# Kernel tuning notes

Measured on AMD Instinct MI355X. Metric: run time of the kernel, lower is better.

## Reference

```python
import jax, jax.numpy as jnp
import numpy as np

LATENT, HIDDEN = 512, 1024


def _gru_cell(x, h, w_ih, w_hh, b_ih, b_hh):
    # PyTorch GRU cell: gates ordered (r, z, n)
    gi = x @ w_ih.T + b_ih          # (B, 3H)
    gh = h @ w_hh.T + b_hh          # (B, 3H)
    i_r, i_z, i_n = jnp.split(gi, 3, axis=-1)
    h_r, h_z, h_n = jnp.split(gh, 3, axis=-1)
    r = jax.nn.sigmoid(i_r + h_r)
    z = jax.nn.sigmoid(i_z + h_z)
    n = jnp.tanh(i_n + r * h_n)
    return (1.0 - z) * n + z * h


def setup_inputs() -> dict:
    key = jax.random.key(0)
    ks = jax.random.split(key, 16)
    B, T_in = 128, 64
    k = 1.0 / np.sqrt(HIDDEN)
    u = lambda kk, shape: jax.random.uniform(kk, shape, jnp.float32, -k, k)
    return {
        "context_latents": jax.random.normal(ks[0], (B, T_in, LATENT), jnp.float32),
        "w_ih_l0": u(ks[1], (3 * HIDDEN, LATENT)),
        "w_hh_l0": u(ks[2], (3 * HIDDEN, HIDDEN)),
        "b_ih_l0": u(ks[3], (3 * HIDDEN,)),
        "b_hh_l0": u(ks[4], (3 * HIDDEN,)),
        "w_ih_l1": u(ks[5], (3 * HIDDEN, HIDDEN)),
        "w_hh_l1": u(ks[6], (3 * HIDDEN, HIDDEN)),
        "b_ih_l1": u(ks[7], (3 * HIDDEN,)),
        "b_hh_l1": u(ks[8], (3 * HIDDEN,)),
        "w1": u(ks[9], (HIDDEN, HIDDEN)),
        "bp1": u(ks[10], (HIDDEN,)),
        "w2": u(ks[11], (LATENT, HIDDEN)),
        "bp2": u(ks[12], (LATENT,)),
        "num_predictions": 64,
    }


def reference(context_latents, w_ih_l0, w_hh_l0, b_ih_l0, b_hh_l0,
              w_ih_l1, w_hh_l1, b_ih_l1, b_hh_l1, w1, bp1, w2, bp2,
              num_predictions):
    B = context_latents.shape[0]
    h0 = jnp.zeros((B, HIDDEN), context_latents.dtype)
    h1 = jnp.zeros((B, HIDDEN), context_latents.dtype)

    def stack(x_t, h0, h1):
        h0 = _gru_cell(x_t, h0, w_ih_l0, w_hh_l0, b_ih_l0, b_hh_l0)
        h1 = _gru_cell(h0, h1, w_ih_l1, w_hh_l1, b_ih_l1, b_hh_l1)
        return h0, h1

    # Encode context: scan over time (B, T_in, D) -> final hidden states
    def enc_step(carry, x_t):
        h0, h1 = carry
        h0, h1 = stack(x_t, h0, h1)
        return (h0, h1), None

    (h0, h1), _ = jax.lax.scan(enc_step, (h0, h1),
                               jnp.swapaxes(context_latents, 0, 1))

    def dec_step(carry, _):
        h0, h1, x = carry
        h0, h1 = stack(x, h0, h1)
        y = jax.nn.relu(h1 @ w1.T + bp1) @ w2.T + bp2   # (B, LATENT)
        return (h0, h1, y), y

    x0 = context_latents[:, -1, :]
    _, ys = jax.lax.scan(dec_step, (h0, h1, x0), None, length=num_predictions)
    return jnp.swapaxes(ys, 0, 1)  # (B, T_out, LATENT)
```

## Files before the change

### kernel.cpp

```cpp
#include <hip/hip_runtime.h>
#include <math.h>

#define B 128
#define LATENT 512
#define H 1024
#define BH (B * H)

typedef unsigned short ushort_t;
typedef unsigned int uint_t;
typedef __bf16 bf16x8 __attribute__((ext_vector_type(8)));
typedef float f32x4 __attribute__((ext_vector_type(4)));


__global__ __launch_bounds__(256) void zero4_kernel(float4* __restrict__ p, int n4) {
  int i = blockIdx.x * blockDim.x + threadIdx.x;
  int stride = gridDim.x * blockDim.x;
  float4 z = {0.f, 0.f, 0.f, 0.f};
  for (; i < n4; i += stride) p[i] = z;
}

__device__ __forceinline__ void split_bf16(float f, ushort_t& h, ushort_t& l) {
  uint_t u = __float_as_uint(f);
  uint_t hb = (u + 0x7FFFu + ((u >> 16) & 1u)) >> 16;
  float fh = __uint_as_float(hb << 16);
  float r = f - fh;
  uint_t v = __float_as_uint(r);
  uint_t lb = (v + 0x7FFFu + ((v >> 16) & 1u)) >> 16;
  h = (ushort_t)hb; l = (ushort_t)lb;
}

__global__ __launch_bounds__(256) void split_kernel(const float* __restrict__ src,
                                                    ushort_t* __restrict__ hi,
                                                    ushort_t* __restrict__ lo, int n) {
  int i = blockIdx.x * blockDim.x + threadIdx.x;
  int stride = gridDim.x * blockDim.x;
  for (; i < n; i += stride) {
    ushort_t h, l;
    split_bf16(src[i], h, l);
    hi[i] = h; lo[i] = l;
  }
}

__global__ __launch_bounds__(256) void split_hi_kernel(const float* __restrict__ src,
                                                       ushort_t* __restrict__ hi, int n) {
  int i = blockIdx.x * blockDim.x + threadIdx.x;
  int stride = gridDim.x * blockDim.x;
  for (; i < n; i += stride) {
    uint_t u = __float_as_uint(src[i]);
    hi[i] = (ushort_t)((u + 0x7FFFu + ((u >> 16) & 1u)) >> 16);
  }
}

__global__ __launch_bounds__(256) void wf_kernel(const float* __restrict__ wih0,
                                                 const float* __restrict__ w2,
                                                 ushort_t* __restrict__ wfh,
                                                 ushort_t* __restrict__ wfl) {
  __shared__ float As[32][33];
  __shared__ float Bs[32][33];
  const int i0 = blockIdx.x * 32;
  const int k0 = blockIdx.y * 32;
  const int tid = threadIdx.x;
  const int r = tid >> 3, c4 = (tid & 7) << 2;
  float acc[4] = {0.f, 0.f, 0.f, 0.f};
  for (int m0 = 0; m0 < LATENT; m0 += 32) {
    {
      const float4 v = *reinterpret_cast<const float4*>(&wih0[(size_t)(i0 + r) * LATENT + m0 + c4]);
      As[r][c4] = v.x; As[r][c4 + 1] = v.y; As[r][c4 + 2] = v.z; As[r][c4 + 3] = v.w;
      const float4 w = *reinterpret_cast<const float4*>(&w2[(size_t)(m0 + r) * H + k0 + c4]);
      Bs[r][c4] = w.x; Bs[r][c4 + 1] = w.y; Bs[r][c4 + 2] = w.z; Bs[r][c4 + 3] = w.w;
    }
    __syncthreads();
    #pragma unroll
    for (int mm = 0; mm < 32; ++mm) {
      const float a = As[r][mm];
      #pragma unroll
      for (int x = 0; x < 4; ++x) acc[x] = fmaf(a, Bs[mm][c4 + x], acc[x]);
    }
    __syncthreads();
  }
  #pragma unroll
  for (int x = 0; x < 4; ++x) {
    ushort_t h, l;
    split_bf16(acc[x], h, l);
    const size_t o = (size_t)(i0 + r) * H + k0 + c4 + x;
    wfh[o] = h; wfl[o] = l;
  }
}

__global__ __launch_bounds__(256) void bias_fuse_kernel(const float* __restrict__ wih0,
                                                        const float* __restrict__ bp2,
                                                        const float* __restrict__ bih0,
                                                        float* __restrict__ bf0) {
  int g = blockIdx.x * blockDim.x + threadIdx.x;
  if (g < 3 * H) {
    float s = bih0[g];
    const float* row = wih0 + (size_t)g * LATENT;
    #pragma unroll 4
    for (int l = 0; l < LATENT; ++l) s = fmaf(row[l], bp2[l], s);
    bf0[g] = s;
  }
}

__device__ __forceinline__ float sigmoidf_(float v) { return 1.0f / (1.0f + expf(-v)); }

__device__ __forceinline__ void grid_barrier(unsigned* bar, int tid, int bid) {
  __syncthreads();
  if (tid == 0) {
    const int g = bid & 7;
    unsigned* arr    = bar + (g << 6);
    unsigned* rel    = bar + 1024 + (g << 6);
    unsigned* master = bar + 2048;
    unsigned gen = __hip_atomic_load(rel, __ATOMIC_RELAXED, __HIP_MEMORY_SCOPE_AGENT);
    unsigned a = __hip_atomic_fetch_add(arr, 1u, __ATOMIC_ACQ_REL, __HIP_MEMORY_SCOPE_AGENT);
    if (a == 31u) {
      __hip_atomic_store(arr, 0u, __ATOMIC_RELAXED, __HIP_MEMORY_SCOPE_AGENT);
      unsigned m = __hip_atomic_fetch_add(master, 1u, __ATOMIC_ACQ_REL, __HIP_MEMORY_SCOPE_AGENT);
      if (m == 7u) {
        __hip_atomic_store(master, 0u, __ATOMIC_RELAXED, __HIP_MEMORY_SCOPE_AGENT);
        #pragma unroll
        for (int i = 0; i < 8; ++i)
          __hip_atomic_fetch_add(bar + 1024 + (i << 6), 1u, __ATOMIC_ACQ_REL, __HIP_MEMORY_SCOPE_AGENT);
      }
    }
    while (__hip_atomic_load(rel, __ATOMIC_RELAXED, __HIP_MEMORY_SCOPE_AGENT) == gen)
      __builtin_amdgcn_s_sleep(1);
    (void)__hip_atomic_load(rel, __ATOMIC_ACQUIRE, __HIP_MEMORY_SCOPE_AGENT);
  }
  __syncthreads();
}

template <int NJ, int NG, int PH, int EPI, bool WLO>
__device__ __forceinline__ void phase_mm(
    char* smem, const int tid, const int Mb, const int jb, const bool active,
    const ushort_t* aAh, const ushort_t* aAl, int aApitch, int K1,
    const ushort_t* wAh, const ushort_t* wAl,
    const ushort_t* aBh, const ushort_t* aBl, int aBpitch, int K2,
    const ushort_t* wBh,
    const float* bih, const float* bhh,
    const float* h_prev, float* h_out,
    ushort_t* out_hi, ushort_t* out_lo, int split_pitch,
    const float* bias, float* out_f32)
{
  if (!active) return;
  constexpr int NW = NJ * NG;
  constexpr int NSLOTA = 4 + NW * (WLO ? 2 : 1);
  constexpr int NSLOTB = 4 + NW;
  constexpr int BUFB = NSLOTA * 4096;
  constexpr int NPG = PH * NW;
  constexpr int CW = NJ * 16;

  const int b0 = Mb * 32;
  const int j0 = jb * CW;
  const int NC1 = K1 >> 7;
  const int NC2 = (PH == 2) ? (K2 >> 7) : 0;
  const int NC = NC1 + NC2;

  const char* g[NSLOTA];
  auto build = [&](const ushort_t* ah, const ushort_t* al, int apitch,
                   const ushort_t* wh, const ushort_t* wl, int K) {
    const int rowt = tid >> 4;
    const int cp = tid & 15;
    const int cc = cp ^ rowt;
    #pragma unroll
    for (int u = 0; u < NSLOTA; ++u) {
      const ushort_t* basep; size_t off;
      if (u < 2)      { basep = ah; off = (size_t)(b0 + u * 16 + rowt) * apitch + cc * 8; }
      else if (u < 4) { basep = al; off = (size_t)(b0 + (u - 2) * 16 + rowt) * apitch + cc * 8; }
      else if (u < 4 + NW) {
        const int w = u - 4, jt = w % NJ, gate = w / NJ;
        const int wrow = (NG == 3) ? (gate * H + j0 + jt * 16 + rowt) : (j0 + jt * 16 + rowt);
        basep = wh; off = (size_t)wrow * K + cc * 8;
      } else {
        const int w = u - 4 - NW, jt = w % NJ, gate = w / NJ;
        const int wrow = (NG == 3) ? (gate * H + j0 + jt * 16 + rowt) : (j0 + jt * 16 + rowt);
        basep = (wl != nullptr) ? wl : wh; off = (size_t)wrow * K + cc * 8;
      }
      g[u] = (const char*)(basep + off);
    }
  };

  const int s = tid >> 6;
  const int q = (tid >> 4) & 3;
  const int r = tid & 15;
  const int gs = (((4 * s + q) ^ r) << 4);
  const int offA00 = r * 256 + gs;
  const int offA01 = 4096 + r * 256 + gs;
  const int offA10 = 8192 + r * 256 + gs;
  const int offA11 = 12288 + r * 256 + gs;
  int offWh[NW];
  int offWl[NW];
  #pragma unroll
  for (int w = 0; w < NW; ++w) {
    offWh[w] = (4 + w) * 4096 + r * 256 + gs;
    offWl[w] = (4 + NW + w) * 4096 + r * 256 + gs;
  }

  f32x4 accA[NJ][NG][2];
  f32x4 accB[NJ][NG][2];
  #pragma unroll
  for (int jt = 0; jt < NJ; ++jt)
    #pragma unroll
    for (int gg = 0; gg < NG; ++gg)
      #pragma unroll
      for (int mf = 0; mf < 2; ++mf) {
        accA[jt][gg][mf] = (f32x4){0.f, 0.f, 0.f, 0.f};
        accB[jt][gg][mf] = (f32x4){0.f, 0.f, 0.f, 0.f};
      }

  const unsigned wofs = (unsigned)(tid >> 6) * 1024;
  auto issue = [&](int bsel, int koff, int nslot) {
    #pragma unroll
    for (int u = 0; u < NSLOTA; ++u) {
      if (u < nslot) {
        __builtin_amdgcn_global_load_lds(
            (const __attribute__((address_space(1))) void*)(g[u] + koff),
            (__attribute__((address_space(3))) void*)(smem + bsel * BUFB + u * 4096 + wofs),
            16, 0, 0);
      }
    }
  };

  auto computeA = [&](int bsel) {
    const char* base = smem + bsel * BUFB;
    bf16x8 ah0 = *(const bf16x8*)(base + offA00);
    bf16x8 ah1 = *(const bf16x8*)(base + offA01);
    bf16x8 al0 = *(const bf16x8*)(base + offA10);
    bf16x8 al1 = *(const bf16x8*)(base + offA11);
    #pragma unroll
    for (int gg = 0; gg < NG; ++gg)
      #pragma unroll
      for (int jt = 0; jt < NJ; ++jt) {
        const int w = gg * NJ + jt;
        bf16x8 wh = *(const bf16x8*)(base + offWh[w]);
        accA[jt][gg][0] = __builtin_amdgcn_mfma_f32_16x16x32_bf16(ah0, wh, accA[jt][gg][0], 0, 0, 0);
        if (WLO) {
          bf16x8 wl = *(const bf16x8*)(base + offWl[w]);
          accA[jt][gg][0] = __builtin_amdgcn_mfma_f32_16x16x32_bf16(ah0, wl, accA[jt][gg][0], 0, 0, 0);
          accA[jt][gg][1] = __builtin_amdgcn_mfma_f32_16x16x32_bf16(ah1, wl, accA[jt][gg][1], 0, 0, 0);
        }
        accA[jt][gg][0] = __builtin_amdgcn_mfma_f32_16x16x32_bf16(al0, wh, accA[jt][gg][0], 0, 0, 0);
        accA[jt][gg][1] = __builtin_amdgcn_mfma_f32_16x16x32_bf16(ah1, wh, accA[jt][gg][1], 0, 0, 0);
        accA[jt][gg][1] = __builtin_amdgcn_mfma_f32_16x16x32_bf16(al1, wh, accA[jt][gg][1], 0, 0, 0);
      }
  };
  auto computeB = [&](int bsel) {
    const char* base = smem + bsel * BUFB;
    bf16x8 ah0 = *(const bf16x8*)(base + offA00);
    bf16x8 ah1 = *(const bf16x8*)(base + offA01);
    bf16x8 al0 = *(const bf16x8*)(base + offA10);
    bf16x8 al1 = *(const bf16x8*)(base + offA11);
    #pragma unroll
    for (int gg = 0; gg < NG; ++gg)
      #pragma unroll
      for (int jt = 0; jt < NJ; ++jt) {
        const int w = gg * NJ + jt;
        bf16x8 wh = *(const bf16x8*)(base + offWh[w]);
        accB[jt][gg][0] = __builtin_amdgcn_mfma_f32_16x16x32_bf16(ah0, wh, accB[jt][gg][0], 0, 0, 0);
        accB[jt][gg][0] = __builtin_amdgcn_mfma_f32_16x16x32_bf16(al0, wh, accB[jt][gg][0], 0, 0, 0);
        accB[jt][gg][1] = __builtin_amdgcn_mfma_f32_16x16x32_bf16(ah1, wh, accB[jt][gg][1], 0, 0, 0);
        accB[jt][gg][1] = __builtin_amdgcn_mfma_f32_16x16x32_bf16(al1, wh, accB[jt][gg][1], 0, 0, 0);
      }
  };

  build(aAh, aAl, aApitch, wAh, wAl, K1);
  issue(0, 0, NSLOTA);

  #pragma unroll 1
  for (int c = 0; c < NC; ++c) {
    __syncthreads();
    if (c + 1 < NC) {
      if (PH == 2 && c + 1 == NC1) {
        build(aBh, aBl, aBpitch, wBh, nullptr, K2);
        issue((c + 1) & 1, 0, NSLOTB);
      } else {
        const bool isB = (PH == 2) && (c + 1 >= NC1);
        const int koff = (isB ? (c + 1 - NC1) : (c + 1)) * 256;
        issue((c + 1) & 1, koff, isB ? NSLOTB : NSLOTA);
      }
    }
    if (PH == 1 || c < NC1) computeA(c & 1);
    else                    computeB(c & 1);
  }
  __syncthreads();

  const int lane = tid & 63;
  #pragma unroll
  for (int gg = 0; gg < NG; ++gg)
    #pragma unroll
    for (int jt = 0; jt < NJ; ++jt)
      #pragma unroll
      for (int mf = 0; mf < 2; ++mf) {
        const int w = gg * NJ + jt;
        *(f32x4*)(smem + (size_t)(((s * NPG + w) * 2 + mf) * 64 + lane) * 16) = accA[jt][gg][mf];
        if (PH == 2)
          *(f32x4*)(smem + (size_t)(((s * NPG + NW + w) * 2 + mf) * 64 + lane) * 16) = accB[jt][gg][mf];
      }
  __syncthreads();

  for (int o = tid; o < 32 * CW; o += 256) {
    const int row = o / CW, c = o % CW;
    const int jt = c >> 4, cr = c & 15;
    const int mf = row >> 4, br = row & 15, qq = br >> 2, rg = br & 3;
    const int ln = cr + qq * 16;
    float v[PH * NG];
    #pragma unroll
    for (int pg = 0; pg < PH * NG; ++pg) {
      const int w = (pg < NG) ? (pg * NJ + jt) : (NW + (pg - NG) * NJ + jt);
      float sum = 0.f;
      #pragma unroll
      for (int ss = 0; ss < 4; ++ss)
        sum += *(const float*)(smem + (size_t)(((ss * NPG + w) * 2 + mf) * 64 + ln) * 16 + rg * 4);
      v[pg] = sum;
    }
    const int bglob = b0 + row, jglob = j0 + c;
// ... 6 lines not shown
      float hn = v[5] + bhh[2 * H + jglob];
      float rr_ = sigmoidf_(ir + hr);
      float zz_ = sigmoidf_(iz + hz);
      float nn_ = tanhf(in_ + rr_ * hn);
      float hp = h_prev[(size_t)bglob * H + jglob];
      float ho = (1.f - zz_) * nn_ + zz_ * hp;
      h_out[(size_t)bglob * H + jglob] = ho;
      ushort_t hb, lb;
      split_bf16(ho, hb, lb);
      out_hi[(size_t)bglob * H + jglob] = hb;
      out_lo[(size_t)bglob * H + jglob] = lb;
    } else if (EPI == 1) {
      float vv = v[0] + bias[jglob];
      vv = fmaxf(vv, 0.f);
      ushort_t hb, lb;
      split_bf16(vv, hb, lb);
      out_hi[(size_t)bglob * split_pitch + jglob] = hb;
      out_lo[(size_t)bglob * split_pitch + jglob] = lb;
    } else {
      float vv = v[0] + bias[jglob];
      const int tt = bglob >> 7, bb2 = bglob & 127;
      out_f32[((size_t)bb2 * split_pitch + tt) * LATENT + jglob] = vv;
    }
  }
  __syncthreads();
}


struct PParams {
  const ushort_t *ctxh, *ctxl;
  const ushort_t *wih0h, *whh0h;
  const ushort_t *wih1h, *whh1h;
  const ushort_t *w1h;
  const ushort_t *wfh, *wfl;
  const float *bih0, *bhh0, *bih1, *bhh1, *bp1;
  const float *bf0;
  float *h0f0, *h0f1, *h1f0, *h1f1;
  ushort_t *h0hi0, *h0lo0, *h0hi1, *h0lo1;
  ushort_t *h1hi0, *h1lo0, *h1hi1, *h1lo1;
  ushort_t *h0Ahi, *h0Alo;
  unsigned* bar;
  int T_in, n_pred, ctx_pitch;
};

__global__ __launch_bounds__(256, 1) void gru_persistent(PParams P) {
  __shared__ char smem[98304];
  const int tid = threadIdx.x;
  const int bid = blockIdx.x;

  float* h0f[2] = {P.h0f0, P.h0f1};
  float* h1f[2] = {P.h1f0, P.h1f1};
  ushort_t* h0hi[2] = {P.h0hi0, P.h0hi1};
  ushort_t* h0lo[2] = {P.h0lo0, P.h0lo1};
  ushort_t* h1hi[2] = {P.h1hi0, P.h1hi1};
  ushort_t* h1lo[2] = {P.h1lo0, P.h1lo1};

  int p0 = 0, p1 = 0;

  const int idx = (bid < 128) ? bid : (bid - 128);
  const int eMb = idx & 3;
  const int ejb = idx >> 2;
  #pragma unroll 1
  for (int p = 0; p <= P.T_in; ++p) {
    const int n0 = p0 ^ 1, n1 = p1 ^ 1;
    if (bid < 128) {
      if (p < P.T_in) {
        const int t = p;
        phase_mm<2, 3, 2, 0, false>(smem, tid, eMb, ejb, true,
            P.ctxh + (size_t)t * LATENT, P.ctxl + (size_t)t * LATENT, P.ctx_pitch, LATENT,
            P.wih0h, nullptr,
            (t == 0) ? P.h0hi0 : P.h0Ahi + (size_t)(t - 1) * BH,
            (t == 0) ? P.h0lo0 : P.h0Alo + (size_t)(t - 1) * BH, H, H, P.whh0h,
            P.bih0, P.bhh0, h0f[p0], h0f[n0],
            P.h0Ahi + (size_t)t * BH, P.h0Alo + (size_t)t * BH, H, nullptr, nullptr);
      }
    } else {
      if (p >= 1) {
        const int t = p - 1;
        phase_mm<2, 3, 2, 0, false>(smem, tid, eMb, ejb, true,
            P.h0Ahi + (size_t)t * BH, P.h0Alo + (size_t)t * BH, H, H,
            P.wih1h, nullptr,
            h1hi[p1], h1lo[p1], H, H, P.whh1h,
            P.bih1, P.bhh1, h1f[p1], h1f[n1],
            h1hi[n1], h1lo[n1], H, nullptr, nullptr);
      }
    }
    grid_barrier(P.bar, tid, bid);
    if (p < P.T_in) p0 = n0;
    if (p >= 1) p1 = n1;
  }

  const int dMb = bid & 3;
  const int djb = bid >> 2;
  const ushort_t* d0ph = P.h0Ahi + (size_t)(P.T_in - 1) * BH;
  const ushort_t* d0pl = P.h0Alo + (size_t)(P.T_in - 1) * BH;
  ushort_t* pAh = P.h0Ahi;
  ushort_t* pAl = P.h0Alo;
  #pragma unroll 1
  for (int t = 0; t < P.n_pred; ++t) {
    const int n0 = p0 ^ 1;
    if (t == 0) {
      phase_mm<1, 3, 2, 0, false>(smem, tid, dMb, djb, true,
          P.ctxh + (size_t)(P.T_in - 1) * LATENT, P.ctxl + (size_t)(P.T_in - 1) * LATENT,
          P.ctx_pitch, LATENT,
          P.wih0h, nullptr,
          d0ph, d0pl, H, H, P.whh0h,
          P.bih0, P.bhh0, h0f[p0], h0f[n0], h0hi[n0], h0lo[n0], H, nullptr, nullptr);
    } else {
      phase_mm<1, 3, 2, 0, true>(smem, tid, dMb, djb, true,
          pAh + (size_t)(t - 1) * BH, pAl + (size_t)(t - 1) * BH, H, H,
          P.wfh, P.wfl,
          d0ph, d0pl, H, H, P.whh0h,
          P.bf0, P.bhh0, h0f[p0], h0f[n0], h0hi[n0], h0lo[n0], H, nullptr, nullptr);
    }
    grid_barrier(P.bar, tid, bid);
    d0ph = h0hi[n0]; d0pl = h0lo[n0];
    const int n1 = p1 ^ 1;
    phase_mm<1, 3, 2, 0, false>(smem, tid, dMb, djb, true,
        h0hi[n0], h0lo[n0], H, H,
        P.wih1h, nullptr,
        h1hi[p1], h1lo[p1], H, H, P.whh1h,
        P.bih1, P.bhh1, h1f[p1], h1f[n1], h1hi[n1], h1lo[n1], H, nullptr, nullptr);
    grid_barrier(P.bar, tid, bid);
    phase_mm<1, 1, 1, 1, false>(smem, tid, dMb, djb, true,
        h1hi[n1], h1lo[n1], H, H,
        P.w1h, nullptr,
        nullptr, nullptr, 0, 0, nullptr,
        nullptr, nullptr, nullptr, nullptr,
        pAh + (size_t)t * BH, pAl + (size_t)t * BH, H, P.bp1, nullptr);
    grid_barrier(P.bar, tid, bid);
    p0 = n0; p1 = n1;
  }
}

__global__ __launch_bounds__(256, 2) void proj_out_kernel(
    const ushort_t* __restrict__ pAh, const ushort_t* __restrict__ pAl,
    const ushort_t* __restrict__ w2h, const float* __restrict__ bp2,
    float* __restrict__ out, int n_pred)
{
  __shared__ char smem[49152];
  const int tid = threadIdx.x;
  const int rt = blockIdx.x >> 4;
  const int ct = blockIdx.x & 15;
  phase_mm<2, 1, 1, 3, false>(smem, tid, rt, ct, true,
      pAh, pAl, H, H,
      w2h, nullptr,
      nullptr, nullptr, 0, 0, nullptr,
      nullptr, nullptr, nullptr, nullptr,
      nullptr, nullptr, n_pred, bp2, out);
}


__global__ __launch_bounds__(256) void gru_cell_kernel(
    const float* __restrict__ x, int xs, int Kih,
    const float* __restrict__ h_prev,
    const float* __restrict__ wih, const float* __restrict__ whh,
    const float* __restrict__ bih, const float* __restrict__ bhh,
    float* __restrict__ h_out)
{
  __shared__ float Xs[32][33];
  __shared__ float Ws[48][33];
  const int tid = threadIdx.x;
  const int b0 = blockIdx.x * 32;
  const int j0 = blockIdx.y * 16;
  const int bg = tid & 15;
  const int jj = tid >> 4;
  const int j = j0 + jj;
  float accA[2][3];
  float accB[2][3];
  #pragma unroll
  for (int g = 0; g < 3; ++g) {
    const float bi = bih[g * H + j];
    const float bh = bhh[g * H + j];
    accA[0][g] = bi; accA[1][g] = bi;
    accB[0][g] = bh; accB[1][g] = bh;
  }
  for (int k0 = 0; k0 < Kih; k0 += 32) {
    {
      const int rr = tid >> 3, c4 = (tid & 7) << 2;
// ... 116 lines not shown
  const float* bhh0 = (const float*)d_in[4];
  const float* wih1 = (const float*)d_in[5];
  const float* whh1 = (const float*)d_in[6];
  const float* bih1 = (const float*)d_in[7];
  const float* bhh1 = (const float*)d_in[8];
  const float* w1   = (const float*)d_in[9];
  const float* bp1  = (const float*)d_in[10];
  const float* w2   = (const float*)d_in[11];
  const float* bp2  = (const float*)d_in[12];

  const int T_in   = in_sizes[0] / (B * LATENT);
  const int n_pred = out_size / (B * LATENT);
  float* out = (float*)d_out;

  size_t cur = 0;
  auto alloc = [&](size_t bytes) -> void* {
    void* p = (char*)d_ws + cur;
    cur += (bytes + 255) & ~(size_t)255;
    return p;
  };
  const int E_wih0 = 3 * H * LATENT, E_whh0 = 3 * H * H;
  const int E_wih1 = 3 * H * H, E_whh1 = 3 * H * H;
  const int E_w1 = H * H, E_w2 = LATENT * H;
  const int E_wf = 3 * H * H;
  const int E_ctx = in_sizes[0];

  ushort_t* wih0h = (ushort_t*)alloc(E_wih0 * 2);
  ushort_t* whh0h = (ushort_t*)alloc(E_whh0 * 2);
  ushort_t* wih1h = (ushort_t*)alloc(E_wih1 * 2);
  ushort_t* whh1h = (ushort_t*)alloc(E_whh1 * 2);
  ushort_t* w1h   = (ushort_t*)alloc(E_w1 * 2);
  ushort_t* w2h   = (ushort_t*)alloc(E_w2 * 2);
  ushort_t* wfh   = (ushort_t*)alloc((size_t)E_wf * 2);
  ushort_t* wfl   = (ushort_t*)alloc((size_t)E_wf * 2);
  ushort_t* ctxh  = (ushort_t*)alloc((size_t)E_ctx * 2);
  ushort_t* ctxl  = (ushort_t*)alloc((size_t)E_ctx * 2);
  ushort_t* h0Ahi = (ushort_t*)alloc((size_t)T_in * BH * 2);
  ushort_t* h0Alo = (ushort_t*)alloc((size_t)T_in * BH * 2);
  float* bf0 = (float*)alloc(3 * H * 4);
  size_t zero_start = cur;
  float* h0f[2]; float* h1f[2];
  ushort_t* h0hi[2]; ushort_t* h0lo[2]; ushort_t* h1hi[2]; ushort_t* h1lo[2];
  h0f[0] = (float*)alloc(BH * 4); h0f[1] = (float*)alloc(BH * 4);
  h1f[0] = (float*)alloc(BH * 4); h1f[1] = (float*)alloc(BH * 4);
  h0hi[0] = (ushort_t*)alloc(BH * 2); h0lo[0] = (ushort_t*)alloc(BH * 2);
  h0hi[1] = (ushort_t*)alloc(BH * 2); h0lo[1] = (ushort_t*)alloc(BH * 2);
  h1hi[0] = (ushort_t*)alloc(BH * 2); h1lo[0] = (ushort_t*)alloc(BH * 2);
  h1hi[1] = (ushort_t*)alloc(BH * 2); h1lo[1] = (ushort_t*)alloc(BH * 2);
  unsigned* bar = (unsigned*)alloc(16384);
  size_t zero_bytes = cur - zero_start;
  size_t required = cur;

  if (ws_size >= required && n_pred <= T_in) {
    auto splitA = [&](const float* s, ushort_t* hi, ushort_t* lo, int n) {
      int blocks = (n + 255) / 256; if (blocks > 2048) blocks = 2048;
      split_kernel<<<blocks, 256, 0, stream>>>(s, hi, lo, n);
    };
    auto splitW = [&](const float* s, ushort_t* hi, int n) {
      int blocks = (n + 255) / 256; if (blocks > 2048) blocks = 2048;
      split_hi_kernel<<<blocks, 256, 0, stream>>>(s, hi, n);
    };
    splitW(wih0, wih0h, E_wih0);
    splitW(whh0, whh0h, E_whh0);
    splitW(wih1, wih1h, E_wih1);
    splitW(whh1, whh1h, E_whh1);
    splitW(w1, w1h, E_w1);
    splitW(w2, w2h, E_w2);
    wf_kernel<<<dim3(3 * H / 32, H / 32), 256, 0, stream>>>(wih0, w2, wfh, wfl);
    bias_fuse_kernel<<<(3 * H + 255) / 256, 256, 0, stream>>>(wih0, bp2, bih0, bf0);
    splitA(ctx, ctxh, ctxl, E_ctx);
    {
      int n4 = (int)(zero_bytes / 16);
      zero4_kernel<<<2048, 256, 0, stream>>>((float4*)((char*)d_ws + zero_start), n4);
    }

    PParams P;
    P.ctxh = ctxh; P.ctxl = ctxl;
    P.wih0h = wih0h; P.whh0h = whh0h;
    P.wih1h = wih1h; P.whh1h = whh1h;
    P.w1h = w1h; P.wfh = wfh; P.wfl = wfl;
    P.bih0 = bih0; P.bhh0 = bhh0; P.bih1 = bih1; P.bhh1 = bhh1; P.bp1 = bp1;
    P.bf0 = bf0;
    P.h0f0 = h0f[0]; P.h0f1 = h0f[1]; P.h1f0 = h1f[0]; P.h1f1 = h1f[1];
    P.h0hi0 = h0hi[0]; P.h0lo0 = h0lo[0]; P.h0hi1 = h0hi[1]; P.h0lo1 = h0lo[1];
    P.h1hi0 = h1hi[0]; P.h1lo0 = h1lo[0]; P.h1hi1 = h1hi[1]; P.h1lo1 = h1lo[1];
    P.h0Ahi = h0Ahi; P.h0Alo = h0Alo;
    P.bar = bar;
    P.T_in = T_in; P.n_pred = n_pred; P.ctx_pitch = T_in * LATENT;

    gru_persistent<<<256, 256, 0, stream>>>(P);

    const int rowtiles = (n_pred * B) / 32;
    proj_out_kernel<<<rowtiles * 16, 256, 0, stream>>>(h0Ahi, h0Alo, w2h, bp2, out, n_pred);
    return;
  }

  float* ws = (float*)d_ws;
  float* h0a = ws;
  float* h0b = h0a + (size_t)BH;
  float* h1a = h0b + (size_t)BH;
  float* h1b = h1a + (size_t)BH;
  float* p   = h1b + (size_t)BH;
  {
    int n4 = (4 * BH) / 4;
    zero4_kernel<<<256, 256, 0, stream>>>((float4*)h0a, n4);
  }
  float* y = p + (size_t)BH;
  float* h0p = h0a; float* h0n = h0b;
  float* h1p = h1a; float* h1n = h1b;
  const dim3 cgrid(4, 64);
  for (int t = 0; t < T_in; ++t) {
    const float* x = ctx + (size_t)t * LATENT;
    gru_cell_kernel<<<cgrid, 256, 0, stream>>>(x, T_in * LATENT, LATENT,
// ... 27 lines not shown
```

Baseline: 6.677 ms.

## Widen decode K-chunks to 256 and drop low-part fused weight

Adds a CHUNKW template parameter so the decoder-phase matmuls stage 256-wide K chunks per pipeline step instead of 128. This halves the number of load/sync iterations per phase and grows the shared buffer to fit. It also removes the bf16 low half of the fused wih0·w2 weight, so layer-0 decode steps issue fewer MFMAs and load less data. The cost is lower precision in the fused-weight path and higher LDS use per block.

```diff
diff --git a/kernel.cpp b/kernel.cpp
--- a/kernel.cpp
+++ b/kernel.cpp
@@ -53,8 +53,7 @@
 
 __global__ __launch_bounds__(256) void wf_kernel(const float* __restrict__ wih0,
                                                  const float* __restrict__ w2,
-                                                 ushort_t* __restrict__ wfh,
-                                                 ushort_t* __restrict__ wfl) {
+                                                 ushort_t* __restrict__ wfh) {
   __shared__ float As[32][33];
   __shared__ float Bs[32][33];
   const int i0 = blockIdx.x * 32;
@@ -80,10 +79,9 @@
   }
   #pragma unroll
   for (int x = 0; x < 4; ++x) {
-    ushort_t h, l;
-    split_bf16(acc[x], h, l);
-    const size_t o = (size_t)(i0 + r) * H + k0 + c4 + x;
-    wfh[o] = h; wfl[o] = l;
+    uint_t u = __float_as_uint(acc[x]);
+    wfh[(size_t)(i0 + r) * H + k0 + c4 + x] =
+        (ushort_t)((u + 0x7FFFu + ((u >> 16) & 1u)) >> 16);
   }
 }
 
@@ -129,7 +127,7 @@
   __syncthreads();
 }
 
-template <int NJ, int NG, int PH, int EPI, bool WLO>
+template <int NJ, int NG, int PH, int EPI, bool WLO, int CHUNKW>
 __device__ __forceinline__ void phase_mm(
     char* smem, const int tid, const int Mb, const int jb, const bool active,
     const ushort_t* aAh, const ushort_t* aAl, int aApitch, int K1,
@@ -142,17 +140,20 @@
     const float* bias, float* out_f32)
 {
   if (!active) return;
+  constexpr int KST = CHUNKW / 128;
+  constexpr int SLOTB = CHUNKW * 32;
   constexpr int NW = NJ * NG;
   constexpr int NSLOTA = 4 + NW * (WLO ? 2 : 1);
   constexpr int NSLOTB = 4 + NW;
-  constexpr int BUFB = NSLOTA * 4096;
+  constexpr int BUFB = NSLOTA * SLOTB;
   constexpr int NPG = PH * NW;
   constexpr int CW = NJ * 16;
+  constexpr int CSHIFT = (CHUNKW == 256) ? 8 : 7;
 
   const int b0 = Mb * 32;
   const int j0 = jb * CW;
-  const int NC1 = K1 >> 7;
-  const int NC2 = (PH == 2) ? (K2 >> 7) : 0;
+  const int NC1 = K1 >> CSHIFT;
+  const int NC2 = (PH == 2) ? (K2 >> CSHIFT) : 0;
   const int NC = NC1 + NC2;
 
   const char* g[NSLOTA];
@@ -182,18 +183,13 @@
   const int s = tid >> 6;
   const int q = (tid >> 4) & 3;
   const int r = tid & 15;
-  const int gs = (((4 * s + q) ^ r) << 4);
-  const int offA00 = r * 256 + gs;
-  const int offA01 = 4096 + r * 256 + gs;
-  const int offA10 = 8192 + r * 256 + gs;
-  const int offA11 = 12288 + r * 256 + gs;
-  int offWh[NW];
-  int offWl[NW];
+  int gsv[KST];
   #pragma unroll
-  for (int w = 0; w < NW; ++w) {
-    offWh[w] = (4 + w) * 4096 + r * 256 + gs;
-    offWl[w] = (4 + NW + w) * 4096 + r * 256 + gs;
-  }
+  for (int k2 = 0; k2 < KST; ++k2) {
+    const int G = s * (4 * KST) + k2 * 4 + q;
+    gsv[k2] = (G >> 4) * 4096 + ((G & 15) ^ r) * 16;
+  }
+  const int rbase = r * 256;
 
   f32x4 accA[NJ][NG][2];
   f32x4 accB[NJ][NG][2];
@@ -212,54 +208,65 @@
     #pragma unroll
     for (int u = 0; u < NSLOTA; ++u) {
       if (u < nslot) {
-        __builtin_amdgcn_global_load_lds(
-            (const __attribute__((address_space(1))) void*)(g[u] + koff),
-            (__attribute__((address_space(3))) void*)(smem + bsel * BUFB + u * 4096 + wofs),
-            16, 0, 0);
+        #pragma unroll
+        for (int j = 0; j < KST; ++j) {
+          __builtin_amdgcn_global_load_lds(
+              (const __attribute__((address_space(1))) void*)(g[u] + koff + j * 256),
+              (__attribute__((address_space(3))) void*)(smem + bsel * BUFB + u * SLOTB + j * 4096 + wofs),
+              16, 0, 0);
+        }
       }
     }
   };
 
   auto computeA = [&](int bsel) {
     const char* base = smem + bsel * BUFB;
-    bf16x8 ah0 = *(const bf16x8*)(base + offA00);
-    bf16x8 ah1 = *(const bf16x8*)(base + offA01);
-    bf16x8 al0 = *(const bf16x8*)(base + offA10);
-    bf16x8 al1 = *(const bf16x8*)(base + offA11);
-    #pragma unroll
-    for (int gg = 0; gg < NG; ++gg)
+    #pragma unroll
+    for (int k2 = 0; k2 < KST; ++k2) {
+      const int fo = rbase + gsv[k2];
+      bf16x8 ah0 = *(const bf16x8*)(base + 0 * SLOTB + fo);
+      bf16x8 ah1 = *(const bf16x8*)(base + 1 * SLOTB + fo);
+      bf16x8 al0 = *(const bf16x8*)(base + 2 * SLOTB + fo);
+      bf16x8 al1 = *(const bf16x8*)(base + 3 * SLOTB + fo);
       #pragma unroll
-      for (int jt = 0; jt < NJ; ++jt) {
-        const int w = gg * NJ + jt;
-        bf16x8 wh = *(const bf16x8*)(base + offWh[w]);
-        accA[jt][gg][0] = __builtin_amdgcn_mfma_f32_16x16x32_bf16(ah0, wh, accA[jt][gg][0], 0, 0, 0);
-        if (WLO) {
-          bf16x8 wl = *(const bf16x8*)(base + offWl[w]);
-          accA[jt][gg][0] = __builtin_amdgcn_mfma_f32_16x16x32_bf16(ah0, wl, accA[jt][gg][0], 0, 0, 0);
-          accA[jt][gg][1] = __builtin_amdgcn_mfma_f32_16x16x32_bf16(ah1, wl, accA[jt][gg][1], 0, 0, 0);
+      for (int gg = 0; gg < NG; ++gg)
+        #pragma unroll
+        for (int jt = 0; jt < NJ; ++jt) {
+          const int w = gg * NJ + jt;
+          bf16x8 wh = *(const bf16x8*)(base + (4 + w) * SLOTB + fo);
+          accA[jt][gg][0] = __builtin_amdgcn_mfma_f32_16x16x32_bf16(ah0, wh, accA[jt][gg][0], 0, 0, 0);
+          if (WLO) {
+            bf16x8 wl = *(const bf16x8*)(base + (4 + NW + w) * SLOTB + fo);
+            accA[jt][gg][0] = __builtin_amdgcn_mfma_f32_16x16x32_bf16(ah0, wl, accA[jt][gg][0], 0, 0, 0);
+            accA[jt][gg][1] = __builtin_amdgcn_mfma_f32_16x16x32_bf16(ah1, wl, accA[jt][gg][1], 0, 0, 0);
+          }
+          accA[jt][gg][0] = __builtin_amdgcn_mfma_f32_16x16x32_bf16(al0, wh, accA[jt][gg][0], 0, 0, 0);
+          accA[jt][gg][1] = __builtin_amdgcn_mfma_f32_16x16x32_bf16(ah1, wh, accA[jt][gg][1], 0, 0, 0);
+          accA[jt][gg][1] = __builtin_amdgcn_mfma_f32_16x16x32_bf16(al1, wh, accA[jt][gg][1], 0, 0, 0);
         }
-        accA[jt][gg][0] = __builtin_amdgcn_mfma_f32_16x16x32_bf16(al0, wh, accA[jt][gg][0], 0, 0, 0);
-        accA[jt][gg][1] = __builtin_amdgcn_mfma_f32_16x16x32_bf16(ah1, wh, accA[jt][gg][1], 0, 0, 0);
-        accA[jt][gg][1] = __builtin_amdgcn_mfma_f32_16x16x32_bf16(al1, wh, accA[jt][gg][1], 0, 0, 0);
-      }
+    }
   };
   auto computeB = [&](int bsel) {
     const char* base = smem + bsel * BUFB;
-    bf16x8 ah0 = *(const bf16x8*)(base + offA00);
-    bf16x8 ah1 = *(const bf16x8*)(base + offA01);
-    bf16x8 al0 = *(const bf16x8*)(base + offA10);
-    bf16x8 al1 = *(const bf16x8*)(base + offA11);
-    #pragma unroll
-    for (int gg = 0; gg < NG; ++gg)
+    #pragma unroll
+    for (int k2 = 0; k2 < KST; ++k2) {
+      const int fo = rbase + gsv[k2];
+      bf16x8 ah0 = *(const bf16x8*)(base + 0 * SLOTB + fo);
+      bf16x8 ah1 = *(const bf16x8*)(base + 1 * SLOTB + fo);
+      bf16x8 al0 = *(const bf16x8*)(base + 2 * SLOTB + fo);
+      bf16x8 al1 = *(const bf16x8*)(base + 3 * SLOTB + fo);
       #pragma unroll
-      for (int jt = 0; jt < NJ; ++jt) {
-        const int w = gg * NJ + jt;
-        bf16x8 wh = *(const bf16x8*)(base + offWh[w]);
-        accB[jt][gg][0] = __builtin_amdgcn_mfma_f32_16x16x32_bf16(ah0, wh, accB[jt][gg][0], 0, 0, 0);
-        accB[jt][gg][0] = __builtin_amdgcn_mfma_f32_16x16x32_bf16(al0, wh, accB[jt][gg][0], 0, 0, 0);
-        accB[jt][gg][1] = __builtin_amdgcn_mfma_f32_16x16x32_bf16(ah1, wh, accB[jt][gg][1], 0, 0, 0);
-        accB[jt][gg][1] = __builtin_amdgcn_mfma_f32_16x16x32_bf16(al1, wh, accB[jt][gg][1], 0, 0, 0);
-      }
+      for (int gg = 0; gg < NG; ++gg)
+        #pragma unroll
+        for (int jt = 0; jt < NJ; ++jt) {
+          const int w = gg * NJ + jt;
+          bf16x8 wh = *(const bf16x8*)(base + (4 + w) * SLOTB + fo);
+          accB[jt][gg][0] = __builtin_amdgcn_mfma_f32_16x16x32_bf16(ah0, wh, accB[jt][gg][0], 0, 0, 0);
+          accB[jt][gg][0] = __builtin_amdgcn_mfma_f32_16x16x32_bf16(al0, wh, accB[jt][gg][0], 0, 0, 0);
+          accB[jt][gg][1] = __builtin_amdgcn_mfma_f32_16x16x32_bf16(ah1, wh, accB[jt][gg][1], 0, 0, 0);
+          accB[jt][gg][1] = __builtin_amdgcn_mfma_f32_16x16x32_bf16(al1, wh, accB[jt][gg][1], 0, 0, 0);
+        }
+    }
   };
 
   build(aAh, aAl, aApitch, wAh, wAl, K1);
@@ -274,7 +281,7 @@
         issue((c + 1) & 1, 0, NSLOTB);
       } else {
         const bool isB = (PH == 2) && (c + 1 >= NC1);
-        const int koff = (isB ? (c + 1 - NC1) : (c + 1)) * 256;
+        const int koff = (isB ? (c + 1 - NC1) : (c + 1)) * (CHUNKW * 2);
         issue((c + 1) & 1, koff, isB ? NSLOTB : NSLOTA);
       }
     }
@@ -352,7 +359,7 @@
   const ushort_t *wih0h, *whh0h;
   const ushort_t *wih1h, *whh1h;
   const ushort_t *w1h;
-  const ushort_t *wfh, *wfl;
+  const ushort_t *wfh;
   const float *bih0, *bhh0, *bih1, *bhh1, *bp1;
   const float *bf0;
   float *h0f0, *h0f1, *h1f0, *h1f1;
@@ -364,7 +371,7 @@
 };
 
 __global__ __launch_bounds__(256, 1) void gru_persistent(PParams P) {
-  __shared__ char smem[98304];
+  __shared__ char smem[114688];
   const int tid = threadIdx.x;
   const int bid = blockIdx.x;
 
@@ -386,7 +393,7 @@
     if (bid < 128) {
       if (p < P.T_in) {
         const int t = p;
-        phase_mm<2, 3, 2, 0, false>(smem, tid, eMb, ejb, true,
+        phase_mm<2, 3, 2, 0, false, 128>(smem, tid, eMb, ejb, true,
             P.ctxh + (size_t)t * LATENT, P.ctxl + (size_t)t * LATENT, P.ctx_pitch, LATENT,
             P.wih0h, nullptr,
             (t == 0) ? P.h0hi0 : P.h0Ahi + (size_t)(t - 1) * BH,
@@ -397,7 +404,7 @@
     } else {
       if (p >= 1) {
         const int t = p - 1;
-        phase_mm<2, 3, 2, 0, false>(smem, tid, eMb, ejb, true,
+        phase_mm<2, 3, 2, 0, false, 128>(smem, tid, eMb, ejb, true,
             P.h0Ahi + (size_t)t * BH, P.h0Alo + (size_t)t * BH, H, H,
             P.wih1h, nullptr,
             h1hi[p1], h1lo[p1], H, H, P.whh1h,
@@ -420,29 +427,29 @@
   for (int t = 0; t < P.n_pred; ++t) {
     const int n0 = p0 ^ 1;
     if (t == 0) {
-      phase_mm<1, 3, 2, 0, false>(smem, tid, dMb, djb, true,
+      phase_mm<1, 3, 2, 0, false, 256>(smem, tid, dMb, djb, true,
           P.ctxh + (size_t)(P.T_in - 1) * LATENT, P.ctxl + (size_t)(P.T_in - 1) * LATENT,
           P.ctx_pitch, LATENT,
           P.wih0h, nullptr,
           d0ph, d0pl, H, H, P.whh0h,
           P.bih0, P.bhh0, h0f[p0], h0f[n0], h0hi[n0], h0lo[n0], H, nullptr, nullptr);
     } else {
-      phase_mm<1, 3, 2, 0, true>(smem, tid, dMb, djb, true,
+      phase_mm<1, 3, 2, 0, false, 256>(smem, tid, dMb, djb, true,
           pAh + (size_t)(t - 1) * BH, pAl + (size_t)(t - 1) * BH, H, H,
-          P.wfh, P.wfl,
+          P.wfh, nullptr,
           d0ph, d0pl, H, H, P.whh0h,
           P.bf0, P.bhh0, h0f[p0], h0f[n0], h0hi[n0], h0lo[n0], H, nullptr, nullptr);
     }
     grid_barrier(P.bar, tid, bid);
     d0ph = h0hi[n0]; d0pl = h0lo[n0];
     const int n1 = p1 ^ 1;
-    phase_mm<1, 3, 2, 0, false>(smem, tid, dMb, djb, true,
+    phase_mm<1, 3, 2, 0, false, 256>(smem, tid, dMb, djb, true,
         h0hi[n0], h0lo[n0], H, H,
         P.wih1h, nullptr,
         h1hi[p1], h1lo[p1], H, H, P.whh1h,
         P.bih1, P.bhh1, h1f[p1], h1f[n1], h1hi[n1], h1lo[n1], H, nullptr, nullptr);
     grid_barrier(P.bar, tid, bid);
-    phase_mm<1, 1, 1, 1, false>(smem, tid, dMb, djb, true,
+    phase_mm<1, 1, 1, 1, false, 256>(smem, tid, dMb, djb, true,
         h1hi[n1], h1lo[n1], H, H,
         P.w1h, nullptr,
         nullptr, nullptr, 0, 0, nullptr,
@@ -462,7 +469,7 @@
   const int tid = threadIdx.x;
   const int rt = blockIdx.x >> 4;
   const int ct = blockIdx.x & 15;
-  phase_mm<2, 1, 1, 3, false>(smem, tid, rt, ct, true,
+  phase_mm<2, 1, 1, 3, false, 128>(smem, tid, rt, ct, true,
       pAh, pAl, H, H,
       w2h, nullptr,
       nullptr, nullptr, 0, 0, nullptr,
@@ -647,7 +654,6 @@
   ushort_t* w1h   = (ushort_t*)alloc(E_w1 * 2);
   ushort_t* w2h   = (ushort_t*)alloc(E_w2 * 2);
   ushort_t* wfh   = (ushort_t*)alloc((size_t)E_wf * 2);
-  ushort_t* wfl   = (ushort_t*)alloc((size_t)E_wf * 2);
   ushort_t* ctxh  = (ushort_t*)alloc((size_t)E_ctx * 2);
   ushort_t* ctxl  = (ushort_t*)alloc((size_t)E_ctx * 2);
   ushort_t* h0Ahi = (ushort_t*)alloc((size_t)T_in * BH * 2);
@@ -681,7 +687,7 @@
     splitW(whh1, whh1h, E_whh1);
     splitW(w1, w1h, E_w1);
     splitW(w2, w2h, E_w2);
-    wf_kernel<<<dim3(3 * H / 32, H / 32), 256, 0, stream>>>(wih0, w2, wfh, wfl);
+    wf_kernel<<<dim3(3 * H / 32, H / 32), 256, 0, stream>>>(wih0, w2, wfh);
     bias_fuse_kernel<<<(3 * H + 255) / 256, 256, 0, stream>>>(wih0, bp2, bih0, bf0);
     splitA(ctx, ctxh, ctxl, E_ctx);
     {
@@ -693,7 +699,7 @@
     P.ctxh = ctxh; P.ctxl = ctxl;
     P.wih0h = wih0h; P.whh0h = whh0h;
     P.wih1h = wih1h; P.whh1h = whh1h;
-    P.w1h = w1h; P.wfh = wfh; P.wfl = wfl;
+    P.w1h = w1h; P.wfh = wfh;
     P.bih0 = bih0; P.bhh0 = bhh0; P.bih1 = bih1; P.bhh1 = bhh1; P.bp1 = bp1;
     P.bf0 = bf0;
     P.h0f0 = h0f[0]; P.h0f1 = h0f[1]; P.h1f0 = h1f[0]; P.h1f1 = h1f[1];
```

New measurement: 6.560 ms. About the same (-1.8%).

## Triple-buffer GEMM loads with vmcnt waits, drop fused-weight low part, remap tiles

Applied to the files above, without the earlier changes.

Replaces the double-buffered, syncthreads-per-chunk load loop in phase_mm with a three-deep ring of global_load_lds buffers. Explicit s_waitcnt vmcnt counts let two chunks of loads stay in flight while the current one is computed. It also drops the bf16 low part of the fused decoder weight (wih0·w2), removing extra MFMAs and loads in the decode layer-0 phase at some accuracy cost. Block-to-tile mapping is changed, likely for L2 locality, and shared memory grows to hold the third buffer.

```diff
diff --git a/kernel.cpp b/kernel.cpp
--- a/kernel.cpp
+++ b/kernel.cpp
@@ -10,6 +10,9 @@
 typedef unsigned int uint_t;
 typedef __bf16 bf16x8 __attribute__((ext_vector_type(8)));
 typedef float f32x4 __attribute__((ext_vector_type(4)));
+
+#define AS1 __attribute__((address_space(1)))
+#define AS3 __attribute__((address_space(3)))
 
 
 __global__ __launch_bounds__(256) void zero4_kernel(float4* __restrict__ p, int n4) {
@@ -53,8 +56,7 @@
 
 __global__ __launch_bounds__(256) void wf_kernel(const float* __restrict__ wih0,
                                                  const float* __restrict__ w2,
-                                                 ushort_t* __restrict__ wfh,
-                                                 ushort_t* __restrict__ wfl) {
+                                                 ushort_t* __restrict__ wfh) {
   __shared__ float As[32][33];
   __shared__ float Bs[32][33];
   const int i0 = blockIdx.x * 32;
@@ -80,10 +82,9 @@
   }
   #pragma unroll
   for (int x = 0; x < 4; ++x) {
-    ushort_t h, l;
-    split_bf16(acc[x], h, l);
-    const size_t o = (size_t)(i0 + r) * H + k0 + c4 + x;
-    wfh[o] = h; wfl[o] = l;
+    uint_t u = __float_as_uint(acc[x]);
+    wfh[(size_t)(i0 + r) * H + k0 + c4 + x] =
+        (ushort_t)((u + 0x7FFFu + ((u >> 16) & 1u)) >> 16);
   }
 }
 
@@ -129,11 +130,13 @@
   __syncthreads();
 }
 
-template <int NJ, int NG, int PH, int EPI, bool WLO>
+#define WAIT_VM(N) asm volatile("s_waitcnt vmcnt(" #N ")" ::: "memory")
+
+template <int NJ, int NG, int PH, int EPI>
 __device__ __forceinline__ void phase_mm(
     char* smem, const int tid, const int Mb, const int jb, const bool active,
     const ushort_t* aAh, const ushort_t* aAl, int aApitch, int K1,
-    const ushort_t* wAh, const ushort_t* wAl,
+    const ushort_t* wAh,
     const ushort_t* aBh, const ushort_t* aBl, int aBpitch, int K2,
     const ushort_t* wBh,
     const float* bih, const float* bhh,
@@ -143,9 +146,8 @@
 {
   if (!active) return;
   constexpr int NW = NJ * NG;
-  constexpr int NSLOTA = 4 + NW * (WLO ? 2 : 1);
-  constexpr int NSLOTB = 4 + NW;
-  constexpr int BUFB = NSLOTA * 4096;
+  constexpr int NSLOT = 4 + NW;
+  constexpr int BUFB = NSLOT * 4096;
   constexpr int NPG = PH * NW;
   constexpr int CW = NJ * 16;
 
@@ -155,29 +157,26 @@
   const int NC2 = (PH == 2) ? (K2 >> 7) : 0;
   const int NC = NC1 + NC2;
 
-  const char* g[NSLOTA];
+  const char* g[NSLOT];
   auto build = [&](const ushort_t* ah, const ushort_t* al, int apitch,
-                   const ushort_t* wh, const ushort_t* wl, int K) {
+                   const ushort_t* wh, int K) {
     const int rowt = tid >> 4;
     const int cp = tid & 15;
     const int cc = cp ^ rowt;
     #pragma unroll
-    for (int u = 0; u < NSLOTA; ++u) {
+    for (int u = 0; u < NSLOT; ++u) {
       const ushort_t* basep; size_t off;
       if (u < 2)      { basep = ah; off = (size_t)(b0 + u * 16 + rowt) * apitch + cc * 8; }
       else if (u < 4) { basep = al; off = (size_t)(b0 + (u - 2) * 16 + rowt) * apitch + cc * 8; }
-      else if (u < 4 + NW) {
+      else {
         const int w = u - 4, jt = w % NJ, gate = w / NJ;
         const int wrow = (NG == 3) ? (gate * H + j0 + jt * 16 + rowt) : (j0 + jt * 16 + rowt);
         basep = wh; off = (size_t)wrow * K + cc * 8;
-      } else {
-        const int w = u - 4 - NW, jt = w % NJ, gate = w / NJ;
-        const int wrow = (NG == 3) ? (gate * H + j0 + jt * 16 + rowt) : (j0 + jt * 16 + rowt);
-        basep = (wl != nullptr) ? wl : wh; off = (size_t)wrow * K + cc * 8;
       }
       g[u] = (const char*)(basep + off);
     }
   };
+  build(aAh, aAl, aApitch, wAh, K1);
 
   const int s = tid >> 6;
   const int q = (tid >> 4) & 3;
@@ -187,13 +186,9 @@
   const int offA01 = 4096 + r * 256 + gs;
   const int offA10 = 8192 + r * 256 + gs;
   const int offA11 = 12288 + r * 256 + gs;
-  int offWh[NW];
-  int offWl[NW];
+  int offW[NW];
   #pragma unroll
-  for (int w = 0; w < NW; ++w) {
-    offWh[w] = (4 + w) * 4096 + r * 256 + gs;
-    offWl[w] = (4 + NW + w) * 4096 + r * 256 + gs;
-  }
+  for (int w = 0; w < NW; ++w) offW[w] = (4 + w) * 4096 + r * 256 + gs;
 
   f32x4 accA[NJ][NG][2];
   f32x4 accB[NJ][NG][2];
@@ -208,20 +203,19 @@
       }
 
   const unsigned wofs = (unsigned)(tid >> 6) * 1024;
-  auto issue = [&](int bsel, int koff, int nslot) {
-    #pragma unroll
-    for (int u = 0; u < NSLOTA; ++u) {
-      if (u < nslot) {
-        __builtin_amdgcn_global_load_lds(
-            (const __attribute__((address_space(1))) void*)(g[u] + koff),
-            (__attribute__((address_space(3))) void*)(smem + bsel * BUFB + u * 4096 + wofs),
-            16, 0, 0);
-      }
-    }
+  auto issue = [&](int cc2) {
+    const bool isB = (PH == 2) && (cc2 >= NC1);
+    const int koff = (isB ? (cc2 - NC1) : cc2) * 256;
+    char* dst = smem + (cc2 % 3) * BUFB + wofs;
+    #pragma unroll
+    for (int u = 0; u < NSLOT; ++u)
+      __builtin_amdgcn_global_load_lds(
+          (const AS1 void*)(g[u] + koff),
+          (AS3 void*)(dst + u * 4096), 16, 0, 0);
   };
 
-  auto computeA = [&](int bsel) {
-    const char* base = smem + bsel * BUFB;
+  auto compute = [&](int slot, f32x4 (&acc)[NJ][NG][2]) {
+    const char* base = smem + slot * BUFB;
     bf16x8 ah0 = *(const bf16x8*)(base + offA00);
     bf16x8 ah1 = *(const bf16x8*)(base + offA01);
     bf16x8 al0 = *(const bf16x8*)(base + offA10);
@@ -231,55 +225,45 @@
       #pragma unroll
       for (int jt = 0; jt < NJ; ++jt) {
         const int w = gg * NJ + jt;
-        bf16x8 wh = *(const bf16x8*)(base + offWh[w]);
-        accA[jt][gg][0] = __builtin_amdgcn_mfma_f32_16x16x32_bf16(ah0, wh, accA[jt][gg][0], 0, 0, 0);
-        if (WLO) {
-          bf16x8 wl = *(const bf16x8*)(base + offWl[w]);
-          accA[jt][gg][0] = __builtin_amdgcn_mfma_f32_16x16x32_bf16(ah0, wl, accA[jt][gg][0], 0, 0, 0);
-          accA[jt][gg][1] = __builtin_amdgcn_mfma_f32_16x16x32_bf16(ah1, wl, accA[jt][gg][1], 0, 0, 0);
-        }
-        accA[jt][gg][0] = __builtin_amdgcn_mfma_f32_16x16x32_bf16(al0, wh, accA[jt][gg][0], 0, 0, 0);
-        accA[jt][gg][1] = __builtin_amdgcn_mfma_f32_16x16x32_bf16(ah1, wh, accA[jt][gg][1], 0, 0, 0);
-        accA[jt][gg][1] = __builtin_amdgcn_mfma_f32_16x16x32_bf16(al1, wh, accA[jt][gg][1], 0, 0, 0);
+        bf16x8 wh = *(const bf16x8*)(base + offW[w]);
+        acc[jt][gg][0] = __builtin_amdgcn_mfma_f32_16x16x32_bf16(ah0, wh, acc[jt][gg][0], 0, 0, 0);
+        acc[jt][gg][0] = __builtin_amdgcn_mfma_f32_16x16x32_bf16(al0, wh, acc[jt][gg][0], 0, 0, 0);
+        acc[jt][gg][1] = __builtin_amdgcn_mfma_f32_16x16x32_bf16(ah1, wh, acc[jt][gg][1], 0, 0, 0);
+        acc[jt][gg][1] = __builtin_amdgcn_mfma_f32_16x16x32_bf16(al1, wh, acc[jt][gg][1], 0, 0, 0);
       }
   };
-  auto computeB = [&](int bsel) {
-    const char* base = smem + bsel * BUFB;
-    bf16x8 ah0 = *(const bf16x8*)(base + offA00);
-    bf16x8 ah1 = *(const bf16x8*)(base + offA01);
-    bf16x8 al0 = *(const bf16x8*)(base + offA10);
-    bf16x8 al1 = *(const bf16x8*)(base + offA11);
-    #pragma unroll
-    for (int gg = 0; gg < NG; ++gg)
-      #pragma unroll
-      for (int jt = 0; jt < NJ; ++jt) {
-        const int w = gg * NJ + jt;
-        bf16x8 wh = *(const bf16x8*)(base + offWh[w]);
-        accB[jt][gg][0] = __builtin_amdgcn_mfma_f32_16x16x32_bf16(ah0, wh, accB[jt][gg][0], 0, 0, 0);
-        accB[jt][gg][0] = __builtin_amdgcn_mfma_f32_16x16x32_bf16(al0, wh, accB[jt][gg][0], 0, 0, 0);
-        accB[jt][gg][1] = __builtin_amdgcn_mfma_f32_16x16x32_bf16(ah1, wh, accB[jt][gg][1], 0, 0, 0);
-        accB[jt][gg][1] = __builtin_amdgcn_mfma_f32_16x16x32_bf16(al1, wh, accB[jt][gg][1], 0, 0, 0);
-      }
-  };
-
-  build(aAh, aAl, aApitch, wAh, wAl, K1);
-  issue(0, 0, NSLOTA);
+
+  issue(0);
+  if (NC > 1) issue(1);
+  if (NC > 2) issue(2);
 
   #pragma unroll 1
   for (int c = 0; c < NC; ++c) {
-    __syncthreads();
-    if (c + 1 < NC) {
-      if (PH == 2 && c + 1 == NC1) {
-        build(aBh, aBl, aBpitch, wBh, nullptr, K2);
-        issue((c + 1) & 1, 0, NSLOTB);
+    {
+      const int rem = NC - 1 - c;
+      if (rem <= 0) {
+        WAIT_VM(0);
+      } else if (rem == 1) {
+        if constexpr (NSLOT == 10)      WAIT_VM(10);
+        else if constexpr (NSLOT == 7)  WAIT_VM(7);
+        else if constexpr (NSLOT == 6)  WAIT_VM(6);
+        else                            WAIT_VM(5);
       } else {
-        const bool isB = (PH == 2) && (c + 1 >= NC1);
-        const int koff = (isB ? (c + 1 - NC1) : (c + 1)) * 256;
-        issue((c + 1) & 1, koff, isB ? NSLOTB : NSLOTA);
-      }
-    }
-    if (PH == 1 || c < NC1) computeA(c & 1);
-    else                    computeB(c & 1);
+        if constexpr (NSLOT == 10)      WAIT_VM(20);
+        else if constexpr (NSLOT == 7)  WAIT_VM(14);
+        else if constexpr (NSLOT == 6)  WAIT_VM(12);
+        else                            WAIT_VM(10);
+      }
+    }
+    __builtin_amdgcn_s_barrier();
+    if (PH == 1 || c < NC1) compute(c % 3, accA);
+    else                    compute(c % 3, accB);
+    if (c + 3 < NC) {
+      asm volatile("s_waitcnt lgkmcnt(0)" ::: "memory");
+      __builtin_amdgcn_s_barrier();
+      if (PH == 2 && c + 3 == NC1) build(aBh, aBl, aBpitch, wBh, K2);
+      issue(c + 3);
+    }
   }
   __syncthreads();
 
@@ -352,7 +336,7 @@
   const ushort_t *wih0h, *whh0h;
   const ushort_t *wih1h, *whh1h;
   const ushort_t *w1h;
-  const ushort_t *wfh, *wfl;
+  const ushort_t *wfh;
   const float *bih0, *bhh0, *bih1, *bhh1, *bp1;
   const float *bf0;
   float *h0f0, *h0f1, *h1f0, *h1f1;
@@ -364,7 +348,7 @@
 };
 
 __global__ __launch_bounds__(256, 1) void gru_persistent(PParams P) {
-  __shared__ char smem[98304];
+  __shared__ char smem[122880];
   const int tid = threadIdx.x;
   const int bid = blockIdx.x;
 
@@ -378,17 +362,17 @@
   int p0 = 0, p1 = 0;
 
   const int idx = (bid < 128) ? bid : (bid - 128);
-  const int eMb = idx & 3;
-  const int ejb = idx >> 2;
+  const int eMb = (idx >> 5) & 3;
+  const int ejb = (idx & 7) * 4 + ((idx >> 3) & 3);
   #pragma unroll 1
   for (int p = 0; p <= P.T_in; ++p) {
     const int n0 = p0 ^ 1, n1 = p1 ^ 1;
     if (bid < 128) {
       if (p < P.T_in) {
         const int t = p;
-        phase_mm<2, 3, 2, 0, false>(smem, tid, eMb, ejb, true,
+        phase_mm<2, 3, 2, 0>(smem, tid, eMb, ejb, true,
             P.ctxh + (size_t)t * LATENT, P.ctxl + (size_t)t * LATENT, P.ctx_pitch, LATENT,
-            P.wih0h, nullptr,
+            P.wih0h,
             (t == 0) ? P.h0hi0 : P.h0Ahi + (size_t)(t - 1) * BH,
             (t == 0) ? P.h0lo0 : P.h0Alo + (size_t)(t - 1) * BH, H, H, P.whh0h,
             P.bih0, P.bhh0, h0f[p0], h0f[n0],
@@ -397,9 +381,9 @@
     } else {
       if (p >= 1) {
         const int t = p - 1;
-        phase_mm<2, 3, 2, 0, false>(smem, tid, eMb, ejb, true,
+        phase_mm<2, 3, 2, 0>(smem, tid, eMb, ejb, true,
             P.h0Ahi + (size_t)t * BH, P.h0Alo + (size_t)t * BH, H, H,
-            P.wih1h, nullptr,
+            P.wih1h,
             h1hi[p1], h1lo[p1], H, H, P.whh1h,
             P.bih1, P.bhh1, h1f[p1], h1f[n1],
             h1hi[n1], h1lo[n1], H, nullptr, nullptr);
@@ -410,8 +394,8 @@
     if (p >= 1) p1 = n1;
   }
 
-  const int dMb = bid & 3;
-  const int djb = bid >> 2;
+  const int dMb = (bid >> 6) & 3;
+  const int djb = (bid & 7) * 8 + ((bid >> 3) & 7);
   const ushort_t* d0ph = P.h0Ahi + (size_t)(P.T_in - 1) * BH;
   const ushort_t* d0pl = P.h0Alo + (size_t)(P.T_in - 1) * BH;
   ushort_t* pAh = P.h0Ahi;
@@ -420,31 +404,31 @@
   for (int t = 0; t < P.n_pred; ++t) {
     const int n0 = p0 ^ 1;
     if (t == 0) {
-      phase_mm<1, 3, 2, 0, false>(smem, tid, dMb, djb, true,
+      phase_mm<1, 3, 2, 0>(smem, tid, dMb, djb, true,
           P.ctxh + (size_t)(P.T_in - 1) * LATENT, P.ctxl + (size_t)(P.T_in - 1) * LATENT,
           P.ctx_pitch, LATENT,
-          P.wih0h, nullptr,
+          P.wih0h,
           d0ph, d0pl, H, H, P.whh0h,
           P.bih0, P.bhh0, h0f[p0], h0f[n0], h0hi[n0], h0lo[n0], H, nullptr, nullptr);
     } else {
-      phase_mm<1, 3, 2, 0, true>(smem, tid, dMb, djb, true,
+      phase_mm<1, 3, 2, 0>(smem, tid, dMb, djb, true,
           pAh + (size_t)(t - 1) * BH, pAl + (size_t)(t - 1) * BH, H, H,
-          P.wfh, P.wfl,
+          P.wfh,
           d0ph, d0pl, H, H, P.whh0h,
           P.bf0, P.bhh0, h0f[p0], h0f[n0], h0hi[n0], h0lo[n0], H, nullptr, nullptr);
     }
     grid_barrier(P.bar, tid, bid);
     d0ph = h0hi[n0]; d0pl = h0lo[n0];
     const int n1 = p1 ^ 1;
-    phase_mm<1, 3, 2, 0, false>(smem, tid, dMb, djb, true,
+    phase_mm<1, 3, 2, 0>(smem, tid, dMb, djb, true,
         h0hi[n0], h0lo[n0], H, H,
-        P.wih1h, nullptr,
+        P.wih1h,
         h1hi[p1], h1lo[p1], H, H, P.whh1h,
         P.bih1, P.bhh1, h1f[p1], h1f[n1], h1hi[n1], h1lo[n1], H, nullptr, nullptr);
     grid_barrier(P.bar, tid, bid);
-    phase_mm<1, 1, 1, 1, false>(smem, tid, dMb, djb, true,
+    phase_mm<1, 1, 1, 1>(smem, tid, dMb, djb, true,
         h1hi[n1], h1lo[n1], H, H,
-        P.w1h, nullptr,
+        P.w1h,
         nullptr, nullptr, 0, 0, nullptr,
         nullptr, nullptr, nullptr, nullptr,
         pAh + (size_t)t * BH, pAl + (size_t)t * BH, H, P.bp1, nullptr);
@@ -458,13 +442,13 @@
     const ushort_t* __restrict__ w2h, const float* __restrict__ bp2,
     float* __restrict__ out, int n_pred)
 {
-  __shared__ char smem[49152];
+  __shared__ char smem[73728];
   const int tid = threadIdx.x;
   const int rt = blockIdx.x >> 4;
   const int ct = blockIdx.x & 15;
-  phase_mm<2, 1, 1, 3, false>(smem, tid, rt, ct, true,
+  phase_mm<2, 1, 1, 3>(smem, tid, rt, ct, true,
       pAh, pAl, H, H,
-      w2h, nullptr,
+      w2h,
       nullptr, nullptr, 0, 0, nullptr,
       nullptr, nullptr, nullptr, nullptr,
       nullptr, nullptr, n_pred, bp2, out);
@@ -647,7 +631,6 @@
   ushort_t* w1h   = (ushort_t*)alloc(E_w1 * 2);
   ushort_t* w2h   = (ushort_t*)alloc(E_w2 * 2);
   ushort_t* wfh   = (ushort_t*)alloc((size_t)E_wf * 2);
-  ushort_t* wfl   = (ushort_t*)alloc((size_t)E_wf * 2);
   ushort_t* ctxh  = (ushort_t*)alloc((size_t)E_ctx * 2);
   ushort_t* ctxl  = (ushort_t*)alloc((size_t)E_ctx * 2);
   ushort_t* h0Ahi = (ushort_t*)alloc((size_t)T_in * BH * 2);
@@ -681,7 +664,7 @@
     splitW(whh1, whh1h, E_whh1);
     splitW(w1, w1h, E_w1);
     splitW(w2, w2h, E_w2);
-    wf_kernel<<<dim3(3 * H / 32, H / 32), 256, 0, stream>>>(wih0, w2, wfh, wfl);
+    wf_kernel<<<dim3(3 * H / 32, H / 32), 256, 0, stream>>>(wih0, w2, wfh);
     bias_fuse_kernel<<<(3 * H + 255) / 256, 256, 0, stream>>>(wih0, bp2, bih0, bf0);
     splitA(ctx, ctxh, ctxl, E_ctx);
     {
@@ -693,7 +676,7 @@
     P.ctxh = ctxh; P.ctxl = ctxl;
     P.wih0h = wih0h; P.whh0h = whh0h;
     P.wih1h = wih1h; P.whh1h = whh1h;
-    P.w1h = w1h; P.wfh = wfh; P.wfl = wfl;
+    P.w1h = w1h; P.wfh = wfh;
     P.bih0 = bih0; P.bhh0 = bhh0; P.bih1 = bih1; P.bhh1 = bhh1; P.bp1 = bp1;
     P.bf0 = bf0;
     P.h0f0 = h0f[0]; P.h0f1 = h0f[1]; P.h1f0 = h1f[0]; P.h1f1 = h1f[1];
```

Result: faster. 6.099 ms (-8.7%).
